# Kernel tuning notes

Measured on AMD Instinct MI355X. Metric: run time of the kernel, lower is better.

Reference implementation:

```python
import jax, jax.numpy as jnp
import numpy as np

B, INDIM, POSDIM, L, H, DE, DV, RECEPT = 2, 256, 256, 2048, 8, 64, 64, 64
LN_EPS = 1e-5


def pos_embedding(dim, length):
    # sin/cos with geometric wavelengths length/(0.8 + 1.2**(i+1)); shape (dim, length)
    dsin = dim // 2
    dcos = dim - dsin
    sin_wl = length / (0.8 + 1.2 ** (jnp.arange(dsin, dtype=jnp.float32) + 1.0))[:, None]
    cos_wl = length / (0.8 + 1.2 ** (jnp.arange(dcos, dtype=jnp.float32) + 1.0))[:, None]
    xpos = jnp.arange(length, dtype=jnp.float32)[None, :]
    two_pi = 2.0 * np.pi
    return jnp.concatenate([jnp.sin(two_pi * xpos / sin_wl), jnp.cos(two_pi * xpos / cos_wl)], axis=0)


def _layernorm(x, g, b):
    # normalize over last axis
    mu = jnp.mean(x, axis=-1, keepdims=True)
    var = jnp.mean((x - mu) ** 2, axis=-1, keepdims=True)
    return (x - mu) / jnp.sqrt(var + LN_EPS) * g + b


def setup_inputs() -> dict:
    key = jax.random.key(0)
    ks = jax.random.split(key, 10)
    s = 0.02
    inp = {
        "x": jax.random.normal(ks[0], (B, INDIM, L), dtype=jnp.float32),
        "Wq": jax.random.normal(ks[1], (H * DE, INDIM + POSDIM), dtype=jnp.float32) * s,
        "Wk": jax.random.normal(ks[2], (H * DE, INDIM + POSDIM), dtype=jnp.float32) * s,
        "Wv": jax.random.normal(ks[3], (H * DV, INDIM + POSDIM), dtype=jnp.float32) * s,
        "Wres": jax.random.normal(ks[4], (DV, INDIM), dtype=jnp.float32) * s,
        "Wc": jax.random.normal(ks[5], (DV, H * DV), dtype=jnp.float32) * s,
        "ln1_g": jnp.ones((DV,), jnp.float32),
        "ln1_b": jnp.zeros((DV,), jnp.float32),
        "W1": jax.random.normal(ks[6], (4 * DV, DV), dtype=jnp.float32) * s,
        "W2": jax.random.normal(ks[7], (DV, 4 * DV), dtype=jnp.float32) * s,
        "ln2_g": jnp.ones((DV,), jnp.float32),
        "ln2_b": jnp.zeros((DV,), jnp.float32),
    }
    return inp


def reference(x, Wq, Wk, Wv, Wres, Wc, ln1_g, ln1_b, W1, W2, ln2_g, ln2_b):
    bsz = x.shape[0]
    # residual projection (1x1 conv == channel matmul)
    residual = jnp.einsum('oi,bil->bol', Wres, x)
    # concat positional embedding along channel dim
    pos = pos_embedding(POSDIM, L)
    xp = jnp.concatenate([x, jnp.broadcast_to(pos[None], (bsz,) + pos.shape)], axis=1)
    # QKV projections -> (B, H, D, L)
    q = jnp.einsum('oi,bil->bol', Wq, xp).reshape(bsz, H, DE, L)
    k = jnp.einsum('oi,bil->bol', Wk, xp).reshape(bsz, H, DE, L)
    v = jnp.einsum('oi,bil->bol', Wv, xp).reshape(bsz, H, DV, L)
    # banded receptive attention: mask*(Q^T K); out-of-band scores are exactly 0 (NOT -inf),
    # matching sum(q.unsqueeze(-2) * mask * k.unsqueeze(-3), -1)
    idx = jnp.arange(L)
    band = (jnp.abs(idx[:, None] - idx[None, :]) <= RECEPT).astype(x.dtype)  # (L, L)
    scores = jnp.einsum('bhdl,bhdm->bhlm', q, k) * band / np.float32(np.sqrt(DE))
    attn = jax.nn.softmax(scores, axis=-1)
    # attn @ V^T, back to (B, H, DV, L), flatten heads
    out = jnp.einsum('bhlm,bhvm->bhvl', attn, v).reshape(bsz, H * DV, L)
    pred = jnp.einsum('oi,bil->bol', Wc, out) + residual
    pred = _layernorm(pred.transpose(0, 2, 1), ln1_g, ln1_b).transpose(0, 2, 1)
    # feedforward (1x1 convs) with exact GELU + residual + layernorm
    res2 = pred
    h = jax.nn.gelu(jnp.einsum('oi,bil->bol', W1, pred), approximate=False)
    pred = jnp.einsum('oi,bil->bol', W2, h) + res2
    pred = _layernorm(pred.transpose(0, 2, 1), ln2_g, ln2_b).transpose(0, 2, 1)
    return pred
```

## Files before the change

kernel.cpp:

```cpp
#include <hip/hip_runtime.h>
#include <cstdint>
#include <cstddef>

#define SEQLEN 2048
#define NBATCH 2
#define NIND   256
#define NPOS   256
#define NCIN   512
#define NH     8
#define NDE    64
#define NDV    64
#define NREC   64

typedef __attribute__((ext_vector_type(8))) short s16x8;
typedef __attribute__((ext_vector_type(4))) float f32x4;

__device__ __forceinline__ unsigned short f2bf(float f) {
  union { float f; unsigned u; } v; v.f = f;
  unsigned r = v.u + 0x7fffu + ((v.u >> 16) & 1u);
  return (unsigned short)(r >> 16);
}

__device__ __forceinline__ void gload16(const unsigned short* g, unsigned short* l) {
  __builtin_amdgcn_global_load_lds(
      (const __attribute__((address_space(1))) unsigned int*)g,
      (__attribute__((address_space(3))) unsigned int*)l, 16, 0, 0);
}

__global__ __launch_bounds__(256) void prep_k(const float* __restrict__ x,
                                              const float* __restrict__ Wq,
                                              const float* __restrict__ Wk,
                                              const float* __restrict__ Wv,
                                              const float* __restrict__ Wc,
                                              const float* __restrict__ Wres,
                                              const float* __restrict__ W1,
                                              const float* __restrict__ W2,
                                              unsigned short* __restrict__ xpt,
                                              unsigned short* __restrict__ wqb,
                                              unsigned short* __restrict__ wkb,
                                              unsigned short* __restrict__ wvb,
                                              unsigned short* __restrict__ wcb,
                                              unsigned short* __restrict__ wresb,
                                              unsigned short* __restrict__ w1b,
                                              unsigned short* __restrict__ w2b,
                                              float* __restrict__ vsum) {
  __shared__ float tile[64][65];
  int blk = blockIdx.x;
  int t = threadIdx.x;
  if (blk < 512) {
    int b = blk >> 8, c0 = ((blk >> 5) & 7) * 64, l0 = (blk & 31) * 64;
    if (c0 < NIND) {
      const float* src = x + ((size_t)b * NIND + c0) * SEQLEN;
      int ll = t & 63, cq = t >> 6;
#pragma unroll
      for (int i = 0; i < 16; ++i) {
        int cl = cq * 16 + i;
        tile[cl][ll] = src[(size_t)cl * SEQLEN + l0 + ll];
      }
      __syncthreads();
      int cl2 = t & 63, lq = t >> 6;
      unsigned short* dst = xpt + ((size_t)b * SEQLEN + l0) * NCIN + c0;
#pragma unroll
      for (int i = 0; i < 16; ++i) {
        int l = lq * 16 + i;
        dst[(size_t)l * NCIN + cl2] = f2bf(tile[cl2][l]);
      }
    } else {
      if (b == 1) return;
      int c = c0 + (t & 63);
      int j = c - NIND;
      int i = (j < NPOS / 2) ? j : j - NPOS / 2;
      const double base = (double)1.2f;
      double p = 1.0;
      for (int tt = 0; tt <= i; ++tt) p *= base;
      float w = 0.8f + (float)p;
      float swl = (float)SEQLEN / w;
      const float two_pi = (float)(2.0 * 3.14159265358979323846);
      int wv = t >> 6;
      unsigned short* dst0 = xpt;
      unsigned short* dst1 = xpt + (size_t)SEQLEN * NCIN;
#pragma unroll
      for (int it = 0; it < 16; ++it) {
        int l = l0 + 16 * wv + it;
        float arg = (two_pi * (float)l) / swl;
        unsigned short val = f2bf((j < NPOS / 2) ? sinf(arg) : cosf(arg));
        dst0[(size_t)l * NCIN + c] = val;
        dst1[(size_t)l * NCIN + c] = val;
      }
    }
  } else if (blk == 1360) {
    ((float4*)vsum)[t] = make_float4(0.f, 0.f, 0.f, 0.f);
  } else {
    const float* in;
    unsigned short* out;
    int idx4;
    if (blk < 1280) {
      int i = (blk - 512) * 256 + t;
      int which = i >> 16;
      idx4 = i & 65535;
      in = (which == 0) ? Wq : ((which == 1) ? Wk : Wv);
      out = (which == 0) ? wqb : ((which == 1) ? wkb : wvb);
    } else if (blk < 1312) { in = Wc;   out = wcb;   idx4 = (blk - 1280) * 256 + t; }
    else if (blk < 1328)   { in = Wres; out = wresb; idx4 = (blk - 1312) * 256 + t; }
    else if (blk < 1344)   { in = W1;   out = w1b;   idx4 = (blk - 1328) * 256 + t; }
    else                   { in = W2;   out = w2b;   idx4 = (blk - 1344) * 256 + t; }
    float4 v = ((const float4*)in)[idx4];
    ((ushort4*)out)[idx4] = make_ushort4(f2bf(v.x), f2bf(v.y), f2bf(v.z), f2bf(v.w));
  }
}

__global__ __launch_bounds__(256) void qkv_gemm_k(const unsigned short* __restrict__ Wqb,
                                                  const unsigned short* __restrict__ Wkb,
                                                  const unsigned short* __restrict__ Wvb,
                                                  const unsigned short* __restrict__ xpt,
                                                  unsigned short* __restrict__ qt,
                                                  unsigned short* __restrict__ kt,
                                                  unsigned short* __restrict__ vb,
                                                  float* __restrict__ vsum) {
  __shared__ alignas(16) unsigned short lds[24576];

  int bz = blockIdx.z;
  int y = blockIdx.y;
  int ysel = y >> 3;
  int m0 = (y & 7) * 64;
  int n0 = blockIdx.x * 128;
  const unsigned short* W = (ysel == 0) ? Wqb : ((ysel == 1) ? Wkb : Wvb);
  const unsigned short* Bg = xpt + (size_t)bz * SEQLEN * NCIN;

  int t = threadIdx.x;
  int w = t >> 6, lane = t & 63, lr = lane & 15, hi = lane >> 4;
  int wm = w >> 1, wn = w & 1;

  int sr = lane >> 3;
  int scs = ((lane & 7) ^ sr) * 8;
  const unsigned short* gA0 = W  + (size_t)(m0 + 16 * w + sr) * 512 + scs;
  const unsigned short* gB0 = Bg + (size_t)(n0 + 32 * w + sr) * 512 + scs;

  int swz = (lr & 7) << 3;

  f32x4 acc[2][4];
#pragma unroll
  for (int i = 0; i < 2; ++i)
#pragma unroll
    for (int j = 0; j < 4; ++j) acc[i][j] = (f32x4){0.f, 0.f, 0.f, 0.f};

  auto stage = [&](int buf, int k0) {
    unsigned short* Ad = lds + buf * 12288 + (16 * w) * 64;
    unsigned short* Bd = lds + buf * 12288 + 4096 + (32 * w) * 64;
    gload16(gA0 + k0,            Ad);
    gload16(gA0 + k0 + 8 * 512,  Ad + 8 * 64);
    gload16(gB0 + k0,            Bd);
    gload16(gB0 + k0 + 8 * 512,  Bd + 8 * 64);
    gload16(gB0 + k0 + 16 * 512, Bd + 16 * 64);
    gload16(gB0 + k0 + 24 * 512, Bd + 24 * 64);
  };
  auto compute = [&](int buf) {
    const unsigned short* Ar = lds + buf * 12288;
    const unsigned short* Br = Ar + 4096;
#pragma unroll
    for (int ks = 0; ks < 2; ++ks) {
      s16x8 af[2], bfv[4];
#pragma unroll
      for (int mt = 0; mt < 2; ++mt)
        af[mt] = *(const s16x8*)&Ar[(32 * wm + 16 * mt + lr) * 64 + ((32 * ks + 8 * hi) ^ swz)];
#pragma unroll
      for (int nt = 0; nt < 4; ++nt)
        bfv[nt] = *(const s16x8*)&Br[(64 * wn + 16 * nt + lr) * 64 + ((32 * ks + 8 * hi) ^ swz)];
#pragma unroll
      for (int mt = 0; mt < 2; ++mt)
#pragma unroll
        for (int nt = 0; nt < 4; ++nt)
          acc[mt][nt] = __builtin_amdgcn_mfma_f32_16x16x32_bf16(af[mt], bfv[nt], acc[mt][nt], 0, 0, 0);
    }
  };

  stage(0, 0);
  stage(1, 64);
#pragma unroll
  for (int it = 0; it < 8; ++it) {
    if (it < 7) {
      asm volatile("s_waitcnt vmcnt(6)" ::: "memory");
    } else {
      asm volatile("s_waitcnt vmcnt(0)" ::: "memory");
    }
    __builtin_amdgcn_s_barrier();
    compute(it & 1);
    __builtin_amdgcn_s_barrier();
    if (it < 6) stage(it & 1, (it + 2) * 64);
  }
  __syncthreads();

  if (ysel == 2) {
#pragma unroll
    for (int mt = 0; mt < 2; ++mt)
#pragma unroll
      for (int reg = 0; reg < 4; ++reg) {
        float p = acc[mt][0][reg] + acc[mt][1][reg] + acc[mt][2][reg] + acc[mt][3][reg];
        p += __shfl_xor(p, 1, 64);
        p += __shfl_xor(p, 2, 64);
        p += __shfl_xor(p, 4, 64);
        p += __shfl_xor(p, 8, 64);
        if (lr == 0)
          atomicAdd(&vsum[bz * 512 + m0 + 32 * wm + 16 * mt + 4 * hi + reg], p);
      }
  }

  if (ysel < 2) {
    unsigned short* Cl = lds;
#pragma unroll
    for (int mt = 0; mt < 2; ++mt)
#pragma unroll
      for (int nt = 0; nt < 4; ++nt) {
        int lloc = 64 * wn + 16 * nt + lr;
        int d0 = 32 * wm + 16 * mt + 4 * hi;
        *(ushort4*)&Cl[lloc * 68 + d0] = make_ushort4(f2bf(acc[mt][nt][0]), f2bf(acc[mt][nt][1]),
                                                      f2bf(acc[mt][nt][2]), f2bf(acc[mt][nt][3]));
      }
    __syncthreads();
    int h = m0 >> 6;
    unsigned short* Cb = ((ysel == 0) ? qt : kt) + ((size_t)(bz * NH + h) * SEQLEN + n0) * 64;
    int rr = t >> 1, cc = (t & 1) * 32;
#pragma unroll
    for (int j = 0; j < 4; ++j)
      *(int4*)&Cb[(size_t)rr * 64 + cc + 8 * j] = *(const int4*)&Cl[rr * 68 + cc + 8 * j];
  } else {
    unsigned short* Cl2 = lds;
#pragma unroll
    for (int mt = 0; mt < 2; ++mt)
#pragma unroll
      for (int nt = 0; nt < 4; ++nt) {
        int lloc = 64 * wn + 16 * nt + lr;
#pragma unroll
        for (int reg = 0; reg < 4; ++reg)
          Cl2[(32 * wm + 16 * mt + 4 * hi + reg) * 132 + lloc] = f2bf(acc[mt][nt][reg]);
      }
    __syncthreads();
    int dd = t >> 2, cc = (t & 3) * 32;
    unsigned short* Vb = vb + ((size_t)(bz * 512 + m0 + dd)) * SEQLEN + n0;
#pragma unroll
    for (int j = 0; j < 4; ++j)
      *(int4*)&Vb[cc + 8 * j] = *(const int4*)&Cl2[dd * 132 + cc + 8 * j];
  }
}

__global__ __launch_bounds__(256) void attn_k(const unsigned short* __restrict__ qt,
                                              const unsigned short* __restrict__ kt,
                                              const unsigned short* __restrict__ vb,
                                              const float* __restrict__ vsum,
                                              unsigned short* __restrict__ attnt) {
  __shared__ alignas(16) unsigned short Ps[64 * 200];
  __shared__ float rowcoef[64];

  int bz = blockIdx.z, hh = blockIdx.y;
  int l0 = blockIdx.x * 64;
  int bh = bz * NH + hh;
  const unsigned short* Qb = qt + (size_t)bh * SEQLEN * 64;
  const unsigned short* Kb = kt + (size_t)bh * SEQLEN * 64;
  const unsigned short* Vp = vb + (size_t)(bz * 512 + hh * 64) * SEQLEN;
  int vsbase = bz * 512 + hh * 64;

  int t = threadIdx.x;
  int w = t >> 6, lane = t & 63, lr = lane & 15, hi = lane >> 4;

  s16x8 a0 = *(const s16x8*)(Qb + ((size_t)(l0 + 16 * w + lr)) * 64 + 8 * hi);
  s16x8 a1 = *(const s16x8*)(Qb + ((size_t)(l0 + 16 * w + lr)) * 64 + 32 + 8 * hi);

  f32x4 sc[12];
#pragma unroll
  for (int ct = 0; ct < 12; ++ct) {
    int m = l0 - 64 + 16 * ct + lr;
    const unsigned short* kp = Kb + (ptrdiff_t)m * 64;
    s16x8 b0 = *(const s16x8*)(kp + 8 * hi);
    s16x8 b1 = *(const s16x8*)(kp + 32 + 8 * hi);
    f32x4 acc = {0.f, 0.f, 0.f, 0.f};
    acc = __builtin_amdgcn_mfma_f32_16x16x32_bf16(a0, b0, acc, 0, 0, 0);
    acc = __builtin_amdgcn_mfma_f32_16x16x32_bf16(a1, b1, acc, 0, 0, 0);
    sc[ct] = acc;
  }

  float rcv[4];
#pragma unroll
  for (int i = 0; i < 4; ++i) {
    int r = 16 * w + 4 * hi + i;
    int l = l0 + r;
    float mx = 0.0f;
    float sv[12];
#pragma unroll
    for (int ct = 0; ct < 12; ++ct) {
      int c = 16 * ct + lr;
      int m = l0 - 64 + c;
      bool ib = (c >= r) && (c <= r + 128) && (m >= 0) && (m < SEQLEN);
      float s = sc[ct][i] * 0.125f;
      sv[ct] = ib ? s : -1e30f;
      mx = ib ? fmaxf(mx, s) : mx;
    }
    mx = fmaxf(mx, __shfl_xor(mx, 1, 64));
    mx = fmaxf(mx, __shfl_xor(mx, 2, 64));
    mx = fmaxf(mx, __shfl_xor(mx, 4, 64));
    mx = fmaxf(mx, __shfl_xor(mx, 8, 64));
    float e0 = expf(-mx);
    float zs = 0.f;
#pragma unroll
    for (int ct = 0; ct < 12; ++ct) {
      float e = (sv[ct] > -1e29f) ? expf(sv[ct] - mx) : 0.0f;
      sv[ct] = e;
      zs += e;
    }
    zs += __shfl_xor(zs, 1, 64);
    zs += __shfl_xor(zs, 2, 64);
    zs += __shfl_xor(zs, 4, 64);
    zs += __shfl_xor(zs, 8, 64);
    int lo = l - NREC; if (lo < 0) lo = 0;
    int hi2 = l + NREC; if (hi2 > SEQLEN - 1) hi2 = SEQLEN - 1;
    float inv = 1.0f / (zs + (float)(SEQLEN - (hi2 - lo + 1)) * e0);
    rcv[i] = e0 * inv;
#pragma unroll
    for (int ct = 0; ct < 12; ++ct)
      sc[ct][i] = (sv[ct] > 0.0f) ? (sv[ct] - e0) * inv : 0.0f;
  }

#pragma unroll
  for (int i = 0; i < 4; ++i) {
    int r = 16 * w + 4 * hi + i;
#pragma unroll
    for (int ct = 0; ct < 12; ++ct)
      Ps[r * 200 + 16 * ct + lr] = f2bf(sc[ct][i]);
  }
  if (lr == 0) {
#pragma unroll
    for (int i = 0; i < 4; ++i) rowcoef[16 * w + 4 * hi + i] = rcv[i];
  }
  __syncthreads();

  s16x8 av[6];
#pragma unroll
  for (int ks = 0; ks < 6; ++ks) {
    int m8 = l0 - 64 + 32 * ks + 8 * hi;
    av[ks] = *(const s16x8*)(Vp + (ptrdiff_t)(16 * w + lr) * SEQLEN + m8);
  }
  float vsv[4];
#pragma unroll
  for (int reg = 0; reg < 4; ++reg) vsv[reg] = vsum[vsbase + 16 * w + 4 * hi + reg];

  unsigned short* Ob = attnt + ((size_t)bz * SEQLEN) * 512 + hh * 64;
#pragma unroll
  for (int nt = 0; nt < 4; ++nt) {
    f32x4 acc = {0.f, 0.f, 0.f, 0.f};
#pragma unroll
    for (int ks = 0; ks < 6; ++ks) {
      s16x8 b = *(const s16x8*)&Ps[(16 * nt + lr) * 200 + 32 * ks + 8 * hi];
      acc = __builtin_amdgcn_mfma_f32_16x16x32_bf16(av[ks], b, acc, 0, 0, 0);
    }
    int l = l0 + 16 * nt + lr;
    float rcf = rowcoef[16 * nt + lr];
    ushort4 o = make_ushort4(f2bf(acc[0] + rcf * vsv[0]), f2bf(acc[1] + rcf * vsv[1]),
                             f2bf(acc[2] + rcf * vsv[2]), f2bf(acc[3] + rcf * vsv[3]));
    *(ushort4*)&Ob[(size_t)l * 512 + 16 * w + 4 * hi] = o;
  }
}

__global__ __launch_bounds__(64) void tail_k(const unsigned short* __restrict__ wcb,
                                             const unsigned short* __restrict__ wresb,
                                             const unsigned short* __restrict__ w1b,
                                             const unsigned short* __restrict__ w2b,
                                             const unsigned short* __restrict__ attnt,
                                             const unsigned short* __restrict__ xpt,
                                             const float* __restrict__ g1v,
                                             const float* __restrict__ b1v,
                                             const float* __restrict__ g2v,
                                             const float* __restrict__ b2v,
                                             float* __restrict__ outp) {
  __shared__ float gs1[64], bs1[64], gs2[64], bs2[64];
  __shared__ alignas(16) unsigned short pw[16][72];
  __shared__ alignas(16) unsigned short hw[16][264];

  int b = blockIdx.y;
  int l0 = blockIdx.x * 16;
  int t = threadIdx.x;
  int lr = t & 15, hi = t >> 4;
  gs1[t] = g1v[t]; bs1[t] = b1v[t]; gs2[t] = g2v[t]; bs2[t] = b2v[t];
  __syncthreads();

  int lloc = lr;
  const unsigned short* brow = attnt + ((size_t)b * SEQLEN + l0 + lloc) * 512;
  const unsigned short* xrow = xpt + ((size_t)b * SEQLEN + l0 + lloc) * 512;

  f32x4 acc[4];
#pragma unroll
  for (int i = 0; i < 4; ++i) acc[i] = (f32x4){0.f, 0.f, 0.f, 0.f};
#pragma unroll
  for (int ks = 0; ks < 16; ++ks) {
    s16x8 bf = *(const s16x8*)(brow + 32 * ks + 8 * hi);
#pragma unroll
    for (int mt = 0; mt < 4; ++mt) {
      s16x8 af = *(const s16x8*)(wcb + (size_t)(16 * mt + lr) * 512 + 32 * ks + 8 * hi);
      acc[mt] = __builtin_amdgcn_mfma_f32_16x16x32_bf16(af, bf, acc[mt], 0, 0, 0);
    }
  }
#pragma unroll
  for (int ks = 0; ks < 8; ++ks) {
    s16x8 bf = *(const s16x8*)(xrow + 32 * ks + 8 * hi);
#pragma unroll
    for (int mt = 0; mt < 4; ++mt) {
      s16x8 af = *(const s16x8*)(wresb + (size_t)(16 * mt + lr) * 256 + 32 * ks + 8 * hi);
      acc[mt] = __builtin_amdgcn_mfma_f32_16x16x32_bf16(af, bf, acc[mt], 0, 0, 0);
    }
  }
  float resid[4][4];
  {
    float sum = 0.f, sq = 0.f;
#pragma unroll
    for (int mt = 0; mt < 4; ++mt)
#pragma unroll
      for (int reg = 0; reg < 4; ++reg) { float v = acc[mt][reg]; sum += v; sq += v * v; }
    sum += __shfl_xor(sum, 16, 64); sq += __shfl_xor(sq, 16, 64);
    sum += __shfl_xor(sum, 32, 64); sq += __shfl_xor(sq, 32, 64);
    float mu = sum * (1.0f / 64.0f);
    float var = sq * (1.0f / 64.0f) - mu * mu;
    float rstd = rsqrtf(var + 1e-5f);
#pragma unroll
    for (int mt = 0; mt < 4; ++mt) {
      float o[4];
#pragma unroll
      for (int reg = 0; reg < 4; ++reg) {
        int m = 16 * mt + 4 * hi + reg;
        o[reg] = (acc[mt][reg] - mu) * rstd * gs1[m] + bs1[m];
        resid[mt][reg] = o[reg];
      }
      *(ushort4*)&pw[lr][16 * mt + 4 * hi] =
          make_ushort4(f2bf(o[0]), f2bf(o[1]), f2bf(o[2]), f2bf(o[3]));
    }
  }
  __syncthreads();

  {
    s16x8 bf0 = *(const s16x8*)&pw[lr][8 * hi];
    s16x8 bf1 = *(const s16x8*)&pw[lr][32 + 8 * hi];
#pragma unroll
    for (int mt = 0; mt < 16; ++mt) {
      s16x8 a0 = *(const s16x8*)(w1b + (size_t)(16 * mt + lr) * 64 + 8 * hi);
      s16x8 a1 = *(const s16x8*)(w1b + (size_t)(16 * mt + lr) * 64 + 32 + 8 * hi);
      f32x4 a2 = {0.f, 0.f, 0.f, 0.f};
      a2 = __builtin_amdgcn_mfma_f32_16x16x32_bf16(a0, bf0, a2, 0, 0, 0);
      a2 = __builtin_amdgcn_mfma_f32_16x16x32_bf16(a1, bf1, a2, 0, 0, 0);
      float v0 = a2[0], v1 = a2[1], v2 = a2[2], v3 = a2[3];
      v0 = 0.5f * v0 * (1.0f + erff(v0 * 0.70710678118654752440f));
      v1 = 0.5f * v1 * (1.0f + erff(v1 * 0.70710678118654752440f));
      v2 = 0.5f * v2 * (1.0f + erff(v2 * 0.70710678118654752440f));
      v3 = 0.5f * v3 * (1.0f + erff(v3 * 0.70710678118654752440f));
      *(ushort4*)&hw[lr][16 * mt + 4 * hi] = make_ushort4(f2bf(v0), f2bf(v1), f2bf(v2), f2bf(v3));
    }
  }
  __syncthreads();

  f32x4 acc3[4];
#pragma unroll
  for (int i = 0; i < 4; ++i) acc3[i] = (f32x4){0.f, 0.f, 0.f, 0.f};
#pragma unroll
  for (int ks = 0; ks < 8; ++ks) {
    s16x8 bf = *(const s16x8*)&hw[lr][32 * ks + 8 * hi];
#pragma unroll
    for (int mt = 0; mt < 4; ++mt) {
      s16x8 af = *(const s16x8*)(w2b + (size_t)(16 * mt + lr) * 256 + 32 * ks + 8 * hi);
      acc3[mt] = __builtin_amdgcn_mfma_f32_16x16x32_bf16(af, bf, acc3[mt], 0, 0, 0);
    }
  }
#pragma unroll
  for (int mt = 0; mt < 4; ++mt)
#pragma unroll
    for (int reg = 0; reg < 4; ++reg) acc3[mt][reg] += resid[mt][reg];
  float sum = 0.f, sq = 0.f;
#pragma unroll
  for (int mt = 0; mt < 4; ++mt)
#pragma unroll
    for (int reg = 0; reg < 4; ++reg) { float v = acc3[mt][reg]; sum += v; sq += v * v; }
  sum += __shfl_xor(sum, 16, 64); sq += __shfl_xor(sq, 16, 64);
  sum += __shfl_xor(sum, 32, 64); sq += __shfl_xor(sq, 32, 64);
  float mu = sum * (1.0f / 64.0f);
  float var = sq * (1.0f / 64.0f) - mu * mu;
  float rstd = rsqrtf(var + 1e-5f);
  float* ob = outp + (size_t)b * 64 * SEQLEN;
  int l = l0 + lloc;
#pragma unroll
  for (int mt = 0; mt < 4; ++mt)
#pragma unroll
    for (int reg = 0; reg < 4; ++reg) {
      int m = 16 * mt + 4 * hi + reg;
      ob[(size_t)m * SEQLEN + l] = (acc3[mt][reg] - mu) * rstd * gs2[m] + bs2[m];
    }
}

extern "C" void kernel_launch(void* const* d_in, const int* in_sizes, int n_in,
                              void* d_out, int out_size, void* d_ws, size_t ws_size,
                              hipStream_t stream) {
  const float* x    = (const float*)d_in[0];
  const float* Wq   = (const float*)d_in[1];
  const float* Wk   = (const float*)d_in[2];
  const float* Wv   = (const float*)d_in[3];
  const float* Wres = (const float*)d_in[4];
  const float* Wc   = (const float*)d_in[5];
  const float* ln1g = (const float*)d_in[6];
  const float* ln1b = (const float*)d_in[7];
  const float* W1   = (const float*)d_in[8];
  const float* W2   = (const float*)d_in[9];
  const float* ln2g = (const float*)d_in[10];
  const float* ln2b = (const float*)d_in[11];

  char* base = (char*)d_ws;
  unsigned short* xpt   = (unsigned short*)base; base += (size_t)2097152 * 2;
  unsigned short* wqb   = (unsigned short*)base; base += (size_t)262144 * 2;
  unsigned short* wkb   = (unsigned short*)base; base += (size_t)262144 * 2;
  unsigned short* wvb   = (unsigned short*)base; base += (size_t)262144 * 2;
  unsigned short* wcb   = (unsigned short*)base; base += (size_t)32768 * 2;
  unsigned short* wresb = (unsigned short*)base; base += (size_t)16384 * 2;
  unsigned short* w1b   = (unsigned short*)base; base += (size_t)16384 * 2;
  unsigned short* w2b   = (unsigned short*)base; base += (size_t)16384 * 2;
  unsigned short* qt    = (unsigned short*)base; base += (size_t)2097152 * 2;
  unsigned short* kt    = (unsigned short*)base; base += (size_t)2097152 * 2;
  unsigned short* vbb   = (unsigned short*)base; base += (size_t)2097152 * 2;
  float* vsum           = (float*)base;          base += (size_t)1024 * 4;
  unsigned short* attnt = (unsigned short*)base; base += (size_t)2097152 * 2;
  float* outp = (float*)d_out;

  prep_k<<<1361, 256, 0, stream>>>(x, Wq, Wk, Wv, Wc, Wres, W1, W2,
                                   xpt, wqb, wkb, wvb, wcb, wresb, w1b, w2b, vsum);
  qkv_gemm_k<<<dim3(16, 24, NBATCH), 256, 0, stream>>>(wqb, wkb, wvb, xpt, qt, kt, vbb, vsum);
  attn_k<<<dim3(32, NH, NBATCH), 256, 0, stream>>>(qt, kt, vbb, vsum, attnt);
  tail_k<<<dim3(128, NBATCH), 64, 0, stream>>>(wcb, wresb, w1b, w2b, attnt, xpt,
                                               ln1g, ln1b, ln2g, ln2b, outp);
}
```

Before: 70.68 us.

## Shrink attention tile to 16 query rows per single-wave block

The attention kernel now handles 16 query rows per 64-thread block instead of 64 rows per 256-thread block, launching four times as many blocks. This cuts band overcompute from 12 to 9 key tiles for QK and from 6 to 5 k-steps for PV, and zero-pads the probability tile tail. The cost is that V and K rows are re-read by more blocks with less reuse. V loads now happen inside the output loop rather than being preloaded.

```diff
diff --git a/kernel.cpp b/kernel.cpp
--- a/kernel.cpp
+++ b/kernel.cpp
@@ -243,16 +243,16 @@
   }
 }
 
-__global__ __launch_bounds__(256) void attn_k(const unsigned short* __restrict__ qt,
-                                              const unsigned short* __restrict__ kt,
-                                              const unsigned short* __restrict__ vb,
-                                              const float* __restrict__ vsum,
-                                              unsigned short* __restrict__ attnt) {
-  __shared__ alignas(16) unsigned short Ps[64 * 200];
-  __shared__ float rowcoef[64];
+__global__ __launch_bounds__(64) void attn_k(const unsigned short* __restrict__ qt,
+                                             const unsigned short* __restrict__ kt,
+                                             const unsigned short* __restrict__ vb,
+                                             const float* __restrict__ vsum,
+                                             unsigned short* __restrict__ attnt) {
+  __shared__ alignas(16) unsigned short Ps[16][168];
+  __shared__ float rowcoef[16];
 
   int bz = blockIdx.z, hh = blockIdx.y;
-  int l0 = blockIdx.x * 64;
+  int l0 = blockIdx.x * 16;
   int bh = bz * NH + hh;
   const unsigned short* Qb = qt + (size_t)bh * SEQLEN * 64;
   const unsigned short* Kb = kt + (size_t)bh * SEQLEN * 64;
@@ -260,14 +260,14 @@
   int vsbase = bz * 512 + hh * 64;
 
   int t = threadIdx.x;
-  int w = t >> 6, lane = t & 63, lr = lane & 15, hi = lane >> 4;
-
-  s16x8 a0 = *(const s16x8*)(Qb + ((size_t)(l0 + 16 * w + lr)) * 64 + 8 * hi);
-  s16x8 a1 = *(const s16x8*)(Qb + ((size_t)(l0 + 16 * w + lr)) * 64 + 32 + 8 * hi);
-
-  f32x4 sc[12];
-#pragma unroll
-  for (int ct = 0; ct < 12; ++ct) {
+  int lr = t & 15, hi = t >> 4;
+
+  s16x8 a0 = *(const s16x8*)(Qb + ((size_t)(l0 + lr)) * 64 + 8 * hi);
+  s16x8 a1 = *(const s16x8*)(Qb + ((size_t)(l0 + lr)) * 64 + 32 + 8 * hi);
+
+  f32x4 sc[9];
+#pragma unroll
+  for (int ct = 0; ct < 9; ++ct) {
     int m = l0 - 64 + 16 * ct + lr;
     const unsigned short* kp = Kb + (ptrdiff_t)m * 64;
     s16x8 b0 = *(const s16x8*)(kp + 8 * hi);
@@ -281,12 +281,12 @@
   float rcv[4];
 #pragma unroll
   for (int i = 0; i < 4; ++i) {
-    int r = 16 * w + 4 * hi + i;
+    int r = 4 * hi + i;
     int l = l0 + r;
     float mx = 0.0f;
-    float sv[12];
-#pragma unroll
-    for (int ct = 0; ct < 12; ++ct) {
+    float sv[9];
+#pragma unroll
+    for (int ct = 0; ct < 9; ++ct) {
       int c = 16 * ct + lr;
       int m = l0 - 64 + c;
       bool ib = (c >= r) && (c <= r + 128) && (m >= 0) && (m < SEQLEN);
@@ -301,7 +301,7 @@
     float e0 = expf(-mx);
     float zs = 0.f;
 #pragma unroll
-    for (int ct = 0; ct < 12; ++ct) {
+    for (int ct = 0; ct < 9; ++ct) {
       float e = (sv[ct] > -1e29f) ? expf(sv[ct] - mx) : 0.0f;
       sv[ct] = e;
       zs += e;
@@ -315,47 +315,42 @@
     float inv = 1.0f / (zs + (float)(SEQLEN - (hi2 - lo + 1)) * e0);
     rcv[i] = e0 * inv;
 #pragma unroll
-    for (int ct = 0; ct < 12; ++ct)
+    for (int ct = 0; ct < 9; ++ct)
       sc[ct][i] = (sv[ct] > 0.0f) ? (sv[ct] - e0) * inv : 0.0f;
   }
 
 #pragma unroll
   for (int i = 0; i < 4; ++i) {
-    int r = 16 * w + 4 * hi + i;
-#pragma unroll
-    for (int ct = 0; ct < 12; ++ct)
-      Ps[r * 200 + 16 * ct + lr] = f2bf(sc[ct][i]);
-  }
+    int r = 4 * hi + i;
+#pragma unroll
+    for (int ct = 0; ct < 9; ++ct)
+      Ps[r][16 * ct + lr] = f2bf(sc[ct][i]);
+  }
+  for (int z = t; z < 16 * 24; z += 64) Ps[z / 24][144 + z % 24] = 0;
   if (lr == 0) {
 #pragma unroll
-    for (int i = 0; i < 4; ++i) rowcoef[16 * w + 4 * hi + i] = rcv[i];
+    for (int i = 0; i < 4; ++i) rowcoef[4 * hi + i] = rcv[i];
   }
   __syncthreads();
 
-  s16x8 av[6];
-#pragma unroll
-  for (int ks = 0; ks < 6; ++ks) {
-    int m8 = l0 - 64 + 32 * ks + 8 * hi;
-    av[ks] = *(const s16x8*)(Vp + (ptrdiff_t)(16 * w + lr) * SEQLEN + m8);
-  }
-  float vsv[4];
-#pragma unroll
-  for (int reg = 0; reg < 4; ++reg) vsv[reg] = vsum[vsbase + 16 * w + 4 * hi + reg];
-
-  unsigned short* Ob = attnt + ((size_t)bz * SEQLEN) * 512 + hh * 64;
-#pragma unroll
-  for (int nt = 0; nt < 4; ++nt) {
+  float rcf = rowcoef[lr];
+  unsigned short* Ob = attnt + ((size_t)bz * SEQLEN + l0 + lr) * 512 + hh * 64;
+#pragma unroll
+  for (int vt = 0; vt < 4; ++vt) {
     f32x4 acc = {0.f, 0.f, 0.f, 0.f};
 #pragma unroll
-    for (int ks = 0; ks < 6; ++ks) {
-      s16x8 b = *(const s16x8*)&Ps[(16 * nt + lr) * 200 + 32 * ks + 8 * hi];
-      acc = __builtin_amdgcn_mfma_f32_16x16x32_bf16(av[ks], b, acc, 0, 0, 0);
-    }
-    int l = l0 + 16 * nt + lr;
-    float rcf = rowcoef[16 * nt + lr];
+    for (int ks = 0; ks < 5; ++ks) {
+      int m8 = l0 - 64 + 32 * ks + 8 * hi;
+      s16x8 av = *(const s16x8*)(Vp + (ptrdiff_t)(16 * vt + lr) * SEQLEN + m8);
+      s16x8 b = *(const s16x8*)&Ps[lr][32 * ks + 8 * hi];
+      acc = __builtin_amdgcn_mfma_f32_16x16x32_bf16(av, b, acc, 0, 0, 0);
+    }
+    float vsv[4];
+#pragma unroll
+    for (int reg = 0; reg < 4; ++reg) vsv[reg] = vsum[vsbase + 16 * vt + 4 * hi + reg];
     ushort4 o = make_ushort4(f2bf(acc[0] + rcf * vsv[0]), f2bf(acc[1] + rcf * vsv[1]),
                              f2bf(acc[2] + rcf * vsv[2]), f2bf(acc[3] + rcf * vsv[3]));
-    *(ushort4*)&Ob[(size_t)l * 512 + 16 * w + 4 * hi] = o;
+    *(ushort4*)&Ob[16 * vt + 4 * hi] = o;
   }
 }
 
@@ -525,7 +520,7 @@
   prep_k<<<1361, 256, 0, stream>>>(x, Wq, Wk, Wv, Wc, Wres, W1, W2,
                                    xpt, wqb, wkb, wvb, wcb, wresb, w1b, w2b, vsum);
   qkv_gemm_k<<<dim3(16, 24, NBATCH), 256, 0, stream>>>(wqb, wkb, wvb, xpt, qt, kt, vbb, vsum);
-  attn_k<<<dim3(32, NH, NBATCH), 256, 0, stream>>>(qt, kt, vbb, vsum, attnt);
+  attn_k<<<dim3(128, NH, NBATCH), 64, 0, stream>>>(qt, kt, vbb, vsum, attnt);
   tail_k<<<dim3(128, NBATCH), 64, 0, stream>>>(wcb, wresb, w1b, w2b, attnt, xpt,
                                                ln1g, ln1b, ln2g, ln2b, outp);
 }
```

Result: no change. 70.61 us, median of 2 (-0.1%).
